# Kernel tuning notes

Hardware: AMD Instinct MI355X
Metric: run time of the kernel (lower is better)

Reference implementation:

```python
import jax, jax.numpy as jnp
import numpy as np

# dims: batch, seq, vocab, hidden, layers, heads, head_dim, intermediate
B, S, V, Hd, L, H, D, I = 2, 1024, 32000, 1024, 4, 16, 64, 4096
THETA = 1e6
EPS = 1e-6
TOPK = S // 2          # sparsity_ratio = 0.5 -> keep half of the keys per head
STD = 0.02
NEG = -1e9


def _ln(x, w, b):
    m = jnp.mean(x, -1, keepdims=True)
    v = jnp.mean((x - m) ** 2, -1, keepdims=True)
    return (x - m) * jax.lax.rsqrt(v + EPS) * w + b


def _rope_tables():
    inv = 1.0 / (THETA ** (np.arange(0, D, 2, dtype=np.float32) / D))
    f = np.arange(S, dtype=np.float32)[:, None] * inv[None, :]   # [S, D/2]
    emb = np.concatenate([f, f], -1)                              # [S, D]
    return jnp.asarray(np.cos(emb)), jnp.asarray(np.sin(emb))


def _rot(x):  # rotate-half, x: [B,H,S,D]
    x1, x2 = jnp.split(x, 2, axis=-1)
    return jnp.concatenate([-x2, x1], -1)


def setup_inputs() -> dict:
    key = jax.random.key(0)
    it = iter(jax.random.split(key, 24))
    p = lambda sh: jax.random.normal(next(it), sh, jnp.float32) * STD
    return {
        "input_ids": jax.random.randint(next(it), (B, S), 0, V, jnp.int32),
        "attention_mask": jnp.ones((B, S), jnp.float32),
        "embed": p((V, Hd)),
        "ln1_w": jnp.ones((L, Hd)), "ln1_b": jnp.zeros((L, Hd)),
        "Wq": p((L, Hd, Hd)), "Wk": p((L, Hd, Hd)),
        "Wv": p((L, Hd, Hd)), "Wo": p((L, Hd, Hd)),
        "Wr": p((L, Hd, H)),
        "ln2_w": jnp.ones((L, Hd)), "ln2_b": jnp.zeros((L, Hd)),
        "W1": p((L, Hd, I)), "b1": jnp.zeros((L, I)),
        "W2": p((L, I, Hd)), "b2": jnp.zeros((L, Hd)),
        "norm_w": jnp.ones((Hd,)), "norm_b": jnp.zeros((Hd,)),
        "lm_head": p((Hd, V)),
    }


def reference(input_ids, attention_mask, embed, ln1_w, ln1_b, Wq, Wk, Wv, Wo,
              Wr, ln2_w, ln2_b, W1, b1, W2, b2, norm_w, norm_b, lm_head):
    cos, sin = _rope_tables()                                   # [S, D]
    mask_add = (1.0 - attention_mask)[:, None, None, :] * NEG   # [B,1,1,S]
    x = embed[input_ids]                                        # [B,S,Hd]
    scale = 1.0 / np.sqrt(D)

    def block(x, p):
        h = _ln(x, p["ln1_w"], p["ln1_b"])
        heads = lambda w: jnp.einsum('bse,ed->bsd', h, w).reshape(B, S, H, D).transpose(0, 2, 1, 3)
        q, k, v = heads(p["Wq"]), heads(p["Wk"]), heads(p["Wv"])  # [B,H,S,D]
        q = q * cos + _rot(q) * sin
        k = k * cos + _rot(k) * sin
        router = jnp.einsum('bse,eh->bhs', h, p["Wr"])            # [B,H,S]
        kth = jax.lax.top_k(router, TOPK)[0][..., -1:]            # [B,H,1]
        bias = jnp.where(router >= kth, jax.nn.log_sigmoid(router), NEG)[:, :, None, :]
        logits = jnp.einsum('bhsd,bhtd->bhst', q, k) * scale + bias + mask_add
        attn = jax.nn.softmax(logits, -1)
        o = jnp.einsum('bhst,bhtd->bhsd', attn, v).transpose(0, 2, 1, 3).reshape(B, S, Hd)
        x = x + jnp.einsum('bse,ed->bsd', o, p["Wo"])
        h2 = _ln(x, p["ln2_w"], p["ln2_b"])
        m = jax.nn.silu(jnp.einsum('bse,ei->bsi', h2, p["W1"]) + p["b1"])
        x = x + jnp.einsum('bsi,ie->bse', m, p["W2"]) + p["b2"]
        return x, None

    layer_params = {"ln1_w": ln1_w, "ln1_b": ln1_b, "Wq": Wq, "Wk": Wk,
                    "Wv": Wv, "Wo": Wo, "Wr": Wr, "ln2_w": ln2_w,
                    "ln2_b": ln2_b, "W1": W1, "b1": b1, "W2": W2, "b2": b2}
    x, _ = jax.lax.scan(block, x, layer_params)
    x = _ln(x, norm_w, norm_b)
    return jnp.einsum('bse,ev->bsv', x, lm_head)   # [B,S,V]
```

## Files before the change

### kernel.cpp

```cpp
#include <hip/hip_runtime.h>
#include <hip/hip_bf16.h>

#define Bdim 2
#define Sdim 1024
#define Vdim 32000
#define HDdim 1024
#define Ldim 4
#define Hdim 16
#define Ddim 64
#define Idim 4096
#define BSdim 2048

typedef __attribute__((ext_vector_type(8))) short bf16x8;
typedef __attribute__((ext_vector_type(4))) float f32x4;

__device__ __forceinline__ unsigned short f2bf(float f) {
    __hip_bfloat16 h = __float2bfloat16(f);
    return *reinterpret_cast<unsigned short*>(&h);
}

#define MFMA16(a, b, c) __builtin_amdgcn_mfma_f32_16x16x32_bf16((a), (b), (c), 0, 0, 0)

#define GLD16(gp, lp)                                                            \
    __builtin_amdgcn_global_load_lds((const __attribute__((address_space(1))) void*)(gp), \
                                     (__attribute__((address_space(3))) void*)(lp), 16, 0, 0)

template <int N>
__device__ __forceinline__ void vwait() {
    if constexpr (N == 2) asm volatile("s_waitcnt vmcnt(2)" ::: "memory");
    else if constexpr (N == 3) asm volatile("s_waitcnt vmcnt(3)" ::: "memory");
    else if constexpr (N == 4) asm volatile("s_waitcnt vmcnt(4)" ::: "memory");
    else if constexpr (N == 6) asm volatile("s_waitcnt vmcnt(6)" ::: "memory");
}

__global__ __launch_bounds__(256) void tables_kernel(float* __restrict__ cosT, float* __restrict__ sinT) {
    int i = blockIdx.x * 256 + threadIdx.x;
    int d = i & 63;
    int s = i >> 6;
    float inv = powf(1.0e6f, -((float)(2 * (d & 31))) / 64.0f);
    float f = (float)s * inv;
    cosT[i] = cosf(f);
    sinT[i] = sinf(f);
}

__global__ __launch_bounds__(256) void embed_kernel(const int* __restrict__ ids, const float* __restrict__ emb,
                                                    float* __restrict__ x) {
    int m = blockIdx.x;
    int tid = threadIdx.x;
    int id = ids[m];
    const float4* src = (const float4*)(emb + (size_t)id * HDdim);
    ((float4*)(x + (size_t)m * HDdim))[tid] = src[tid];
}

__global__ __launch_bounds__(256) void ln_kernel(const float* __restrict__ x, const float* __restrict__ w,
                                                 const float* __restrict__ bw, unsigned short* __restrict__ outH,
                                                 const float* __restrict__ Wr, float* __restrict__ routerO) {
    int m = blockIdx.x;
    int tid = threadIdx.x;
    float4 a = ((const float4*)(x + (size_t)m * HDdim))[tid];
    float s = a.x + a.y + a.z + a.w;
    #pragma unroll
    for (int o = 1; o < 64; o <<= 1) s += __shfl_xor(s, o);
    __shared__ float red[4], red2[4];
    if ((tid & 63) == 0) red[tid >> 6] = s;
    __syncthreads();
    float mean = (red[0] + red[1] + red[2] + red[3]) * (1.0f / 1024.0f);
    float dx = a.x - mean, dy = a.y - mean, dz = a.z - mean, dw = a.w - mean;
    float s2 = dx * dx + dy * dy + dz * dz + dw * dw;
    #pragma unroll
    for (int o = 1; o < 64; o <<= 1) s2 += __shfl_xor(s2, o);
    if ((tid & 63) == 0) red2[tid >> 6] = s2;
    __syncthreads();
    float var = (red2[0] + red2[1] + red2[2] + red2[3]) * (1.0f / 1024.0f);
    float rs = rsqrtf(var + 1e-6f);
    float4 wv = ((const float4*)w)[tid];
    float4 bv = ((const float4*)bw)[tid];
    float v0 = dx * rs * wv.x + bv.x;
    float v1 = dy * rs * wv.y + bv.y;
    float v2 = dz * rs * wv.z + bv.z;
    float v3 = dw * rs * wv.w + bv.w;
    short4 st = make_short4((short)f2bf(v0), (short)f2bf(v1), (short)f2bf(v2), (short)f2bf(v3));
    *(short4*)(outH + (size_t)m * HDdim + tid * 4) = st;

    if (Wr) {
        __shared__ float rbuf[256][16];
        __shared__ float pbuf[16][17];
        float part[16];
        const float* wr0 = Wr + (size_t)(tid * 4) * Hdim;
        #pragma unroll
        for (int h = 0; h < 16; h++)
            part[h] = v0 * wr0[h] + v1 * wr0[16 + h] + v2 * wr0[32 + h] + v3 * wr0[48 + h];
        #pragma unroll
        for (int h4 = 0; h4 < 4; h4++)
            *(float4*)&rbuf[tid][h4 * 4] = make_float4(part[h4 * 4], part[h4 * 4 + 1], part[h4 * 4 + 2], part[h4 * 4 + 3]);
        __syncthreads();
        {
            int h = tid & 15, g = tid >> 4;
            float sgr = 0.0f;
            #pragma unroll
            for (int i = 0; i < 16; i++) sgr += rbuf[g * 16 + i][h];
            pbuf[g][h] = sgr;
        }
        __syncthreads();
        if (tid < 16) {
            float tot = 0.0f;
            #pragma unroll
            for (int g = 0; g < 16; g++) tot += pbuf[g][tid];
            int b = m >> 10, sI = m & 1023;
            routerO[((size_t)(b * Hdim + tid)) * Sdim + sI] = tot;
        }
    }
}

__global__ __launch_bounds__(1024) void topk_kernel(const float* __restrict__ router, const float* __restrict__ amask,
                                                    float* __restrict__ biasC, int* __restrict__ idxC,
                                                    int* __restrict__ ntA) {
    int bh = blockIdx.x;
    int t = threadIdx.x;
    __shared__ float r[1024];
    __shared__ float kths;
    __shared__ int wcnt[16];
    float v = router[(size_t)bh * Sdim + t];
    r[t] = v;
    __syncthreads();
    int gt = 0, eq = 0;
    for (int j = 0; j < 1024; j++) {
        float xv = r[j];
        gt += (xv > v) ? 1 : 0;
        eq += (xv == v) ? 1 : 0;
    }
    if (gt < 512 && gt + eq >= 512) kths = v;
    biasC[(size_t)bh * Sdim + t] = -1e9f;
    idxC[(size_t)bh * Sdim + t] = 0;
    __syncthreads();
    float kth = kths;
    bool sel = (v >= kth);
    unsigned long long m = __ballot(sel);
    int wid = t >> 6, lane = t & 63;
    if (lane == 0) wcnt[wid] = __popcll(m);
    __syncthreads();
    int base = 0;
    for (int w = 0; w < wid; w++) base += wcnt[w];
    if (sel) {
        int rank = base + (int)__popcll(m & ((1ull << lane) - 1ull));
        float bias = (v >= 0.0f) ? -log1pf(expf(-v)) : (v - log1pf(expf(v)));
        int b = bh >> 4;
        bias += (1.0f - amask[b * Sdim + t]) * (-1e9f);
        biasC[(size_t)bh * Sdim + rank] = bias;
        idxC[(size_t)bh * Sdim + rank] = t;
    }
    if (t == 0) {
        int tot = 0;
        #pragma unroll
        for (int w = 0; w < 16; w++) tot += wcnt[w];
        ntA[bh] = (tot + 63) >> 6;
    }
}

__global__ __launch_bounds__(256) void tconv_kernel(const float* __restrict__ S0,
                                                    unsigned short* __restrict__ D, int K, int ldS) {
    __shared__ float t[32][33];
    int kt = blockIdx.y * 32, nt = blockIdx.x * 32;
    int r = threadIdx.x >> 3, c4 = (threadIdx.x & 7) * 4;
    float4 v = *(const float4*)(S0 + (size_t)(kt + r) * ldS + nt + c4);
    t[r][c4] = v.x; t[r][c4 + 1] = v.y; t[r][c4 + 2] = v.z; t[r][c4 + 3] = v.w;
    __syncthreads();
    short4 o = make_short4((short)f2bf(t[c4][r]), (short)f2bf(t[c4 + 1][r]),
                           (short)f2bf(t[c4 + 2][r]), (short)f2bf(t[c4 + 3][r]));
    *(short4*)(D + (size_t)(nt + r) * K + kt + c4) = o;
}

__global__ __launch_bounds__(256) void tconv_layer(const float* __restrict__ Wq, const float* __restrict__ Wk,
                                                   const float* __restrict__ Wv, const float* __restrict__ Wo,
                                                   const float* __restrict__ W1, const float* __restrict__ W2,
                                                   unsigned short* __restrict__ wts) {
    const size_t M1 = 1u << 20;
    int bid = blockIdx.x;
    const float* S;
    unsigned short* D;
    int K, ldS, nt, kt;
    if (bid < 4096) {
        int z = bid >> 10, t = bid & 1023;
        S = (z == 0) ? Wq : (z == 1) ? Wk : (z == 2) ? Wv : Wo;
        D = wts + (size_t)z * M1;
        K = 1024; ldS = 1024; nt = t & 31; kt = t >> 5;
    } else if (bid < 8192) {
        int t = bid - 4096;
        S = W1; D = wts + 4 * M1;
        K = 1024; ldS = 4096; nt = t % 128; kt = t / 128;
    } else {
        int t = bid - 8192;
        S = W2; D = wts + 8 * M1;
        K = 4096; ldS = 1024; nt = t % 32; kt = t / 32;
    }
    __shared__ float tb[32][33];
    int ktb = kt * 32, ntb = nt * 32;
    int r = threadIdx.x >> 3, c4 = (threadIdx.x & 7) * 4;
    float4 v = *(const float4*)(S + (size_t)(ktb + r) * ldS + ntb + c4);
    tb[r][c4] = v.x; tb[r][c4 + 1] = v.y; tb[r][c4 + 2] = v.z; tb[r][c4 + 3] = v.w;
    __syncthreads();
    short4 o = make_short4((short)f2bf(tb[c4][r]), (short)f2bf(tb[c4 + 1][r]),
                           (short)f2bf(tb[c4 + 2][r]), (short)f2bf(tb[c4 + 3][r]));
    *(short4*)(D + (size_t)(ntb + r) * K + ktb + c4) = o;
}

__global__ __launch_bounds__(256) void kvgather_kernel(const unsigned short* __restrict__ k16,
                                                       const unsigned short* __restrict__ v16,
                                                       const int* __restrict__ idxC, const int* __restrict__ ntA,
                                                       unsigned short* __restrict__ kc,
                                                       unsigned short* __restrict__ vTc) {
    int jt = blockIdx.x;
    int bh = blockIdx.y;
    if (jt >= ntA[bh]) return;
    __shared__ unsigned short T[64][72];
    int tid = threadIdx.x;
    int jl = tid >> 2;
    int part = tid & 3;
    int j = jt * 64 + jl;
    int src = idxC[(size_t)bh * Sdim + j];
    const unsigned short* kr = k16 + ((size_t)bh * Sdim + src) * Ddim + part * 16;
    bf16x8 k0 = *(const bf16x8*)kr;
    bf16x8 k1 = *(const bf16x8*)(kr + 8);
    int swj = (j & 7) << 3;
    unsigned short* kd = kc + ((size_t)bh * Sdim + j) * Ddim;
    *(bf16x8*)(kd + ((part * 16) ^ swj)) = k0;
    *(bf16x8*)(kd + ((part * 16 + 8) ^ swj)) = k1;
    const unsigned short* vr = v16 + ((size_t)bh * Sdim + src) * Ddim + part * 16;
    *(bf16x8*)&T[jl][part * 16] = *(const bf16x8*)vr;
    *(bf16x8*)&T[jl][part * 16 + 8] = *(const bf16x8*)(vr + 8);
    __syncthreads();
    int d = tid >> 2;
    int xr = (d & 7) << 3;
    unsigned short* dst = vTc + ((size_t)bh * Ddim + d) * Sdim + jt * 64;
    #pragma unroll
    for (int cc = 0; cc < 2; cc++) {
        int tb = (tid & 3) * 16 + cc * 8;
        bf16x8 o;
        #pragma unroll
        for (int i = 0; i < 8; i++) o[i] = (short)T[tb + i][d];
        *(bf16x8*)(dst + (tb ^ xr)) = o;
    }
}

template <int EPI, int BM, int BN, int WM, int WN>
__global__ __launch_bounds__(512) void gemm8p(
    const unsigned short* __restrict__ A, const unsigned short* __restrict__ Bt,
    float* __restrict__ OF, unsigned short* __restrict__ Hq, unsigned short* __restrict__ Hk,
    unsigned short* __restrict__ Hv, const float* __restrict__ bias,
    const float* __restrict__ cosT, const float* __restrict__ sinT,
    int Kc, int ldK, int ldC, int gridM, int gridN) {
    constexpr int MI = BM / WM / 16, NI = BN / WN / 16;
    constexpr int MH = MI / 2, NH = NI / 2;
    constexpr int LA = BM / 128, LB = BN / 128;
    constexpr int HA = BM / WM / 2;
    constexpr int HB = BN / WN / 2;
    constexpr int ABUF = BM * 64, BBUF = BN * 64;

    __shared__ unsigned short lds[2 * ABUF + 2 * BBUF];

    int bid = blockIdx.x;
    const int nwg = gridDim.x;
    if ((nwg & 7) == 0) bid = (bid & 7) * (nwg >> 3) + (bid >> 3);
    const int mn = gridM * gridN;
    const int ks = bid / mn;
    const int rem = bid - ks * mn;
    const int bm = (rem % gridM) * BM;
    const int bn = (rem / gridM) * BN;
    const unsigned short* Ap = A + (size_t)ks * Kc;
    const unsigned short* Bp = Bt + (size_t)ks * Kc;

    const int tid = threadIdx.x;
    const int lane = tid & 63, wid = tid >> 6;
    const int lc = lane & 15, lg = lane >> 4;
    const int wwm = wid / WN, wwn = wid % WN;

    const int srow = tid >> 3;
    const int scol = ((tid & 7) ^ (srow & 7)) * 8;
    const int ak0 = (lg * 8) ^ ((lc & 7) * 8);
    const int ak1 = (32 + lg * 8) ^ ((lc & 7) * 8);

    f32x4 acc[MI][NI];
    f32x4 zero = {0.0f, 0.0f, 0.0f, 0.0f};
    #pragma unroll
    for (int i = 0; i < MI; i++)
        #pragma unroll
        for (int j = 0; j < NI; j++) acc[i][j] = zero;

    bf16x8 a[MH][2], b0[NH][2], b1[NH][2];

    auto stage_a = [&](int half, int nbuf, int kt) {
        #pragma unroll
        for (int j = 0; j < LA; j++) {
            const int idx = j * 64 + srow;
            const int grow = (idx / HA) * (BM / WM) + half * HA + (idx % HA);
            const unsigned short* g = Ap + (size_t)(bm + grow) * ldK + kt + scol;
            GLD16(g, &lds[nbuf * ABUF + half * (ABUF / 2) + (j * 512 + tid) * 8]);
        }
    };
    auto stage_b = [&](int half, int nbuf, int kt) {
        #pragma unroll
        for (int j = 0; j < LB; j++) {
            const int idx = j * 64 + srow;
            const int grow = (idx / HB) * (BN / WN) + half * HB + (idx % HB);
            const unsigned short* g = Bp + (size_t)(bn + grow) * ldK + kt + scol;
            GLD16(g, &lds[2 * ABUF + nbuf * BBUF + half * (BBUF / 2) + (j * 512 + tid) * 8]);
        }
    };

#define DS_A(mh_, cur_)                                                                   \
    _Pragma("unroll") for (int m = 0; m < MH; m++) {                                      \
        const int ro = (cur_)*ABUF + (mh_) * (ABUF / 2) + (wwm * HA + m * 16 + lc) * 64;  \
        a[m][0] = *(const bf16x8*)&lds[ro + ak0];                                         \
        a[m][1] = *(const bf16x8*)&lds[ro + ak1];                                         \
    }
#define DS_B(bb_, nh_, cur_)                                                              \
    _Pragma("unroll") for (int n = 0; n < NH; n++) {                                      \
        const int ro = 2 * ABUF + (cur_)*BBUF + (nh_) * (BBUF / 2) + (wwn * HB + n * 16 + lc) * 64; \
        bb_[n][0] = *(const bf16x8*)&lds[ro + ak0];                                       \
        bb_[n][1] = *(const bf16x8*)&lds[ro + ak1];                                       \
    }
#define MFMA_PH(mh_, nh_, bb_)                                                            \
    __builtin_amdgcn_s_setprio(1);                                                        \
    _Pragma("unroll") for (int m = 0; m < MH; m++) _Pragma("unroll") for (int n = 0; n < NH; n++) { \
        acc[(mh_)*MH + m][(nh_)*NH + n] = MFMA16(a[m][0], bb_[n][0], acc[(mh_)*MH + m][(nh_)*NH + n]); \
        acc[(mh_)*MH + m][(nh_)*NH + n] = MFMA16(a[m][1], bb_[n][1], acc[(mh_)*MH + m][(nh_)*NH + n]); \
    }                                                                                     \
    __builtin_amdgcn_s_setprio(0);
#define BAR_PRE()                                                                         \
    __builtin_amdgcn_sched_barrier(0);                                                    \
    __builtin_amdgcn_s_barrier();
#define BAR_END()                                                                         \
    asm volatile("" ::: "memory");                                                        \
    __builtin_amdgcn_s_barrier();                                                         \
    __builtin_amdgcn_sched_barrier(0);

    stage_a(0, 0, 0);
    stage_b(0, 0, 0);
    stage_b(1, 0, 0);
    stage_a(1, 0, 0);
    vwait<LA + LB>();
    BAR_END();

    const int NT = Kc >> 6;
    for (int t = 0; t < NT; t++) {
        const int cur = t & 1, nxt = cur ^ 1;
        const int ktn = (t + 1 < NT) ? (t + 1) * 64 : t * 64;
        DS_A(0, cur);
        DS_B(b0, 0, cur);
        stage_a(0, nxt, ktn);
        BAR_PRE();
        MFMA_PH(0, 0, b0);
        vwait<2 * LA>();
        BAR_END();
        DS_B(b1, 1, cur);
        stage_b(0, nxt, ktn);
        BAR_PRE();
        MFMA_PH(0, 1, b1);
        vwait<LA + LB>();
        BAR_END();
        DS_A(1, cur);
        stage_b(1, nxt, ktn);
        BAR_PRE();
        MFMA_PH(1, 1, b1);
        BAR_END();
        stage_a(1, nxt, ktn);
        BAR_PRE();
        MFMA_PH(1, 0, b0);
        vwait<LA + LB>();
        BAR_END();
    }
    asm volatile("s_waitcnt vmcnt(0)" ::: "memory");
#undef DS_A
#undef DS_B
#undef MFMA_PH
#undef BAR_PRE
#undef BAR_END

    #pragma unroll
    for (int i = 0; i < MI; i++) {
        if (EPI == 1) {
            const int colbase = bn + wwn * (BN / WN);
            const int zc = colbase >> 10;
            unsigned short* OH = (zc == 0) ? Hq : (zc == 1) ? Hk : Hv;
            const int hcol = (colbase >> 6) & 15;
            #pragma unroll
            for (int r = 0; r < 4; r++) {
                int row = bm + wwm * (BM / WM) + i * 16 + lg * 4 + r;
                int b = row >> 10, s = row & 1023;
                size_t base = ((size_t)(b * Hdim + hcol) * Sdim + s) << 6;
                if (zc == 2) {
                    #pragma unroll
                    for (int j = 0; j < 4; j++) OH[base + j * 16 + lc] = f2bf(acc[i][j][r]);
                } else {
                    #pragma unroll
                    for (int j = 0; j < 2; j++) {
                        int d = j * 16 + lc;
                        float x1 = acc[i][j][r];
                        float x2 = acc[i][j + 2][r];
                        float c = cosT[s * 64 + d];
                        float sn = sinT[s * 64 + d];
                        OH[base + d] = f2bf(x1 * c - x2 * sn);
                        OH[base + d + 32] = f2bf(x2 * c + x1 * sn);
                    }
                }
            }
        } else {
            #pragma unroll
            for (int r = 0; r < 4; r++) {
                int row = bm + wwm * (BM / WM) + i * 16 + lg * 4 + r;
                #pragma unroll
                for (int j = 0; j < NI; j++) {
                    int col = bn + wwn * (BN / WN) + j * 16 + lc;
                    float v = acc[i][j][r];
                    if (EPI == 3) {
                        float t = v + bias[col];
                        Hq[(size_t)row * ldC + col] = f2bf(t / (1.0f + expf(-t)));
                    } else if (EPI == 6) {
                        if (ks == 0 && bias != nullptr) v += bias[col];
                        unsafeAtomicAdd(&OF[(size_t)row * ldC + col], v);
                    } else {
                        OF[(size_t)row * ldC + col] = v;
                    }
                }
            }
        }
    }
}

__global__ __launch_bounds__(256) void attn_kernel(const unsigned short* __restrict__ q16,
                                                   const unsigned short* __restrict__ kc,
                                                   const unsigned short* __restrict__ vTc,
                                                   const float* __restrict__ biasC,
                                                   const int* __restrict__ ntA,
                                                   unsigned short* __restrict__ o16) {
    const int qb = blockIdx.x;
    const int bh = blockIdx.y;
    const int tid = threadIdx.x;
    const int w = tid >> 6, lane = tid & 63;
    const int lg = lane >> 4, lc = lane & 15;
    const int nt = ntA[bh];

    __shared__ unsigned short Ks[2][64 * 64];
    __shared__ unsigned short Vs[2][64 * 64];
    __shared__ unsigned short Pq[4][16][72];
    __shared__ float sbAll[1024];

    {
        const float4 bv = ((const float4*)(biasC + (size_t)bh * Sdim))[tid];
        *(float4*)&sbAll[tid * 4] = bv;
    }

    const int qrow = qb * 64 + w * 16 + lc;
    const unsigned short* qbase = q16 + ((size_t)bh * Sdim + qrow) * Ddim;
    bf16x8 qf[2];
    qf[0] = *(const bf16x8*)(qbase + lg * 8);
    qf[1] = *(const bf16x8*)(qbase + 32 + lg * 8);

    const int grow = tid >> 3;
    const int gc = (tid & 7) * 8;
    const unsigned short* kbase = kc + (size_t)bh * Sdim * Ddim;
    const unsigned short* vbase = vTc + (size_t)bh * Ddim * Sdim;

    {
        const unsigned short* kg = kbase + (size_t)grow * Ddim + gc;
        GLD16(kg, &Ks[0][tid * 8]);
        GLD16(kg + 32 * Ddim, &Ks[0][2048 + tid * 8]);
        const unsigned short* vg = vbase + (size_t)grow * Sdim + gc;
        GLD16(vg, &Vs[0][tid * 8]);
        GLD16(vg + 32 * Sdim, &Vs[0][2048 + tid * 8]);
    }
    __syncthreads();

    float m_i = -1e30f, l_i = 0.0f;
    f32x4 ot[4];
    f32x4 zero = {0.0f, 0.0f, 0.0f, 0.0f};
    #pragma unroll
    for (int fd = 0; fd < 4; fd++) ot[fd] = zero;

    const int sw = (lc & 7) << 3;

    for (int tt = 0; tt < nt; tt++) {
        const int cur = tt & 1;
        if (tt > 0) {
            asm volatile("s_waitcnt vmcnt(0)" ::: "memory");
            __builtin_amdgcn_sched_barrier(0);
            __builtin_amdgcn_s_barrier();
        }
        if (tt < nt - 1) {
            const int t1 = (tt + 1) * 64;
            const unsigned short* kg = kbase + (size_t)(t1 + grow) * Ddim + gc;
            GLD16(kg, &Ks[cur ^ 1][tid * 8]);
            GLD16(kg + 32 * Ddim, &Ks[cur ^ 1][2048 + tid * 8]);
            const unsigned short* vg = vbase + (size_t)grow * Sdim + t1 + gc;
            GLD16(vg, &Vs[cur ^ 1][tid * 8]);
            GLD16(vg + 32 * Sdim, &Vs[cur ^ 1][2048 + tid * 8]);
        }

        f32x4 sf[4];
        #pragma unroll
        for (int f = 0; f < 4; f++) {
            const int trow = f * 16 + lc;
            f32x4 a = zero;
            #pragma unroll
            for (int ks = 0; ks < 2; ks++) {
                bf16x8 kfr = *(bf16x8*)&Ks[cur][trow * 64 + ((ks * 32 + lg * 8) ^ sw)];
                a = MFMA16(kfr, qf[ks], a);
            }
            sf[f] = a;
        }
        const int t0 = tt * 64;
        float tmax = -1e30f;
        #pragma unroll
        for (int f = 0; f < 4; f++)
            #pragma unroll
            for (int j = 0; j < 4; j++) {
                float v = sf[f][j] * 0.125f + sbAll[t0 + f * 16 + lg * 4 + j];
                sf[f][j] = v;
                tmax = fmaxf(tmax, v);
            }
        tmax = fmaxf(tmax, __shfl_xor(tmax, 16));
        tmax = fmaxf(tmax, __shfl_xor(tmax, 32));
        float mnew = fmaxf(m_i, tmax);
        float alpha = expf(m_i - mnew);
        float lsum = 0.0f;
        #pragma unroll
        for (int f = 0; f < 4; f++)
            #pragma unroll
            for (int j = 0; j < 4; j++) {
                float p = expf(sf[f][j] - mnew);
                sf[f][j] = p;
                lsum += p;
            }
        lsum += __shfl_xor(lsum, 16);
        lsum += __shfl_xor(lsum, 32);
        l_i = l_i * alpha + lsum;
        m_i = mnew;
        #pragma unroll
        for (int fd = 0; fd < 4; fd++)
            #pragma unroll
            for (int j = 0; j < 4; j++) ot[fd][j] *= alpha;
        #pragma unroll
        for (int f = 0; f < 4; f++) {
            short4 ps = make_short4((short)f2bf(sf[f][0]), (short)f2bf(sf[f][1]),
                                    (short)f2bf(sf[f][2]), (short)f2bf(sf[f][3]));
            *(short4*)&Pq[w][lc][f * 16 + lg * 4] = ps;
        }
        #pragma unroll
        for (int ks = 0; ks < 2; ks++) {
            bf16x8 pf = *(bf16x8*)&Pq[w][lc][ks * 32 + lg * 8];
            #pragma unroll
            for (int fd = 0; fd < 4; fd++) {
                bf16x8 vfr = *(bf16x8*)&Vs[cur][(fd * 16 + lc) * 64 + ((ks * 32 + lg * 8) ^ sw)];
                ot[fd] = MFMA16(vfr, pf, ot[fd]);
            }
        }
    }
    asm volatile("s_waitcnt vmcnt(0)" ::: "memory");
    float rl = 1.0f / l_i;
    int b = bh >> 4, h = bh & 15;
    #pragma unroll
    for (int fd = 0; fd < 4; fd++)
        #pragma unroll
        for (int j = 0; j < 4; j++) {
            int d = fd * 16 + lg * 4 + j;
            o16[((size_t)b * Sdim + qrow) * HDdim + h * 64 + d] = f2bf(ot[fd][j] * rl);
        }
}

extern "C" void kernel_launch(void* const* d_in, const int* in_sizes, int n_in,
                              void* d_out, int out_size, void* d_ws, size_t ws_size,
                              hipStream_t stream) {
    const int* ids = (const int*)d_in[0];
    const float* amask = (const float*)d_in[1];
    const float* emb = (const float*)d_in[2];
    const float* ln1w = (const float*)d_in[3];
    const float* ln1b = (const float*)d_in[4];
    const float* Wq = (const float*)d_in[5];
    const float* Wk = (const float*)d_in[6];
    const float* Wv = (const float*)d_in[7];
    const float* Wo = (const float*)d_in[8];
    const float* Wr = (const float*)d_in[9];
    const float* ln2w = (const float*)d_in[10];
    const float* ln2b = (const float*)d_in[11];
    const float* W1 = (const float*)d_in[12];
    const float* b1 = (const float*)d_in[13];
    const float* W2 = (const float*)d_in[14];
    const float* b2 = (const float*)d_in[15];
    const float* nw = (const float*)d_in[16];
    const float* nb = (const float*)d_in[17];
    const float* lmh = (const float*)d_in[18];
    float* out = (float*)d_out;

    char* p = (char*)d_ws;
    size_t off = 0;
    auto alloc = [&](size_t bytes) -> void* {
        void* r = p + off;
        off += (bytes + 255) & ~(size_t)255;
        return r;
    };
    float* cosT = (float*)alloc((size_t)Sdim * Ddim * 4);
    float* sinT = (float*)alloc((size_t)Sdim * Ddim * 4);
    float* x = (float*)alloc((size_t)BSdim * HDdim * 4);
    unsigned short* h16 = (unsigned short*)alloc((size_t)BSdim * HDdim * 2);
    unsigned short* o16 = (unsigned short*)alloc((size_t)BSdim * HDdim * 2);
    unsigned short* m16 = (unsigned short*)alloc((size_t)BSdim * Idim * 2);
    unsigned short* q16 = (unsigned short*)alloc((size_t)Bdim * Hdim * Sdim * Ddim * 2);
    unsigned short* k16 = (unsigned short*)alloc((size_t)Bdim * Hdim * Sdim * Ddim * 2);
    unsigned short* v16 = (unsigned short*)alloc((size_t)Bdim * Hdim * Sdim * Ddim * 2);
    unsigned short* kcs = (unsigned short*)alloc((size_t)Bdim * Hdim * Sdim * Ddim * 2);
    unsigned short* vTc = (unsigned short*)alloc((size_t)Bdim * Hdim * Sdim * Ddim * 2);
    float* router = (float*)alloc((size_t)Bdim * Hdim * Sdim * 4);
    float* biasC = (float*)alloc((size_t)Bdim * Hdim * Sdim * 4);
    int* idxC = (int*)alloc((size_t)Bdim * Hdim * Sdim * 4);
    int* ntA = (int*)alloc((size_t)Bdim * Hdim * 4);
    unsigned short* wts = (unsigned short*)alloc((size_t)Vdim * HDdim * 2);

    const size_t M1 = 1u << 20;

    tables_kernel<<<256, 256, 0, stream>>>(cosT, sinT);
    embed_kernel<<<BSdim, 256, 0, stream>>>(ids, emb, x);

    for (int l = 0; l < Ldim; l++) {
        const float* Wq_l = Wq + (size_t)l * HDdim * HDdim;
        const float* Wk_l = Wk + (size_t)l * HDdim * HDdim;
        const float* Wv_l = Wv + (size_t)l * HDdim * HDdim;
        const float* Wo_l = Wo + (size_t)l * HDdim * HDdim;
        const float* Wr_l = Wr + (size_t)l * HDdim * Hdim;
        const float* W1_l = W1 + (size_t)l * HDdim * Idim;
        const float* W2_l = W2 + (size_t)l * Idim * HDdim;
        const float* b1_l = b1 + (size_t)l * Idim;
        const float* b2_l = b2 + (size_t)l * HDdim;

        tconv_layer<<<12288, 256, 0, stream>>>(Wq_l, Wk_l, Wv_l, Wo_l, W1_l, W2_l, wts);

        ln_kernel<<<BSdim, 256, 0, stream>>>(x, ln1w + l * HDdim, ln1b + l * HDdim, h16, Wr_l, router);
        topk_kernel<<<Bdim * Hdim, 1024, 0, stream>>>(router, amask, biasC, idxC, ntA);
        gemm8p<1, 128, 128, 4, 2><<<384, 512, 0, stream>>>(h16, wts, nullptr, q16, k16, v16,
                                                           nullptr, cosT, sinT, HDdim, HDdim, 0, 16, 24);
        kvgather_kernel<<<dim3(16, 32), 256, 0, stream>>>(k16, v16, idxC, ntA, kcs, vTc);
        attn_kernel<<<dim3(16, 32), 256, 0, stream>>>(q16, kcs, vTc, biasC, ntA, o16);
        gemm8p<6, 128, 128, 4, 2><<<256, 512, 0, stream>>>(o16, wts + 3 * M1, x, nullptr, nullptr, nullptr,
                                                           nullptr, nullptr, nullptr, 512, HDdim, HDdim, 16, 8);
        ln_kernel<<<BSdim, 256, 0, stream>>>(x, ln2w + l * HDdim, ln2b + l * HDdim, h16, nullptr, nullptr);
        gemm8p<3, 128, 128, 4, 2><<<512, 512, 0, stream>>>(h16, wts + 4 * M1, nullptr, m16, nullptr, nullptr,
                                                           b1_l, nullptr, nullptr, HDdim, HDdim, Idim, 16, 32);
        gemm8p<6, 128, 128, 4, 2><<<512, 512, 0, stream>>>(m16, wts + 8 * M1, x, nullptr, nullptr, nullptr,
                                                           b2_l, nullptr, nullptr, 1024, Idim, HDdim, 16, 8);
    }

    ln_kernel<<<BSdim, 256, 0, stream>>>(x, nw, nb, h16, nullptr, nullptr);
    tconv_kernel<<<dim3(1000, 32, 1), 256, 0, stream>>>(lmh, wts, HDdim, Vdim);
    gemm8p<5, 128, 128, 4, 2><<<4000, 512, 0, stream>>>(h16, wts, out, nullptr, nullptr, nullptr,
                                                        nullptr, nullptr, nullptr, HDdim, HDdim, Vdim, 16, 250);
}
```

Baseline: 1.036 ms.

## Batch weight conversion, gather K inside attention, enlarge LM-head GEMM tiles

All per-layer weight transposes and the lm_head transpose now run up front as one batched conversion into a per-layer buffer, so the per-layer tconv launches are gone. The K gather is folded into the attention kernel, which loads selected key rows by index straight into LDS, so the separate compacted K copy is no longer written and re-read. The LM-head GEMM switches to 256x256 tiles with a 2x4 wave layout. The new buffer costs extra memory, and the bigger tiles may hurt occupancy or register pressure.

```diff
diff --git a/kernel.cpp b/kernel.cpp
--- a/kernel.cpp
+++ b/kernel.cpp
@@ -170,27 +170,29 @@
     *(short4*)(D + (size_t)(nt + r) * K + kt + c4) = o;
 }
 
-__global__ __launch_bounds__(256) void tconv_layer(const float* __restrict__ Wq, const float* __restrict__ Wk,
-                                                   const float* __restrict__ Wv, const float* __restrict__ Wo,
-                                                   const float* __restrict__ W1, const float* __restrict__ W2,
-                                                   unsigned short* __restrict__ wts) {
+__global__ __launch_bounds__(256) void tconv_all(const float* __restrict__ Wq, const float* __restrict__ Wk,
+                                                 const float* __restrict__ Wv, const float* __restrict__ Wo,
+                                                 const float* __restrict__ W1, const float* __restrict__ W2,
+                                                 unsigned short* __restrict__ wtsL) {
     const size_t M1 = 1u << 20;
     int bid = blockIdx.x;
+    int lid = bid / 12288, sub = bid - lid * 12288;
+    unsigned short* wl = wtsL + (size_t)lid * 12 * M1;
     const float* S;
     unsigned short* D;
     int K, ldS, nt, kt;
-    if (bid < 4096) {
-        int z = bid >> 10, t = bid & 1023;
-        S = (z == 0) ? Wq : (z == 1) ? Wk : (z == 2) ? Wv : Wo;
-        D = wts + (size_t)z * M1;
+    if (sub < 4096) {
+        int z = sub >> 10, t = sub & 1023;
+        S = ((z == 0) ? Wq : (z == 1) ? Wk : (z == 2) ? Wv : Wo) + (size_t)lid * M1;
+        D = wl + (size_t)z * M1;
         K = 1024; ldS = 1024; nt = t & 31; kt = t >> 5;
-    } else if (bid < 8192) {
-        int t = bid - 4096;
-        S = W1; D = wts + 4 * M1;
+    } else if (sub < 8192) {
+        int t = sub - 4096;
+        S = W1 + (size_t)lid * 4 * M1; D = wl + 4 * M1;
         K = 1024; ldS = 4096; nt = t % 128; kt = t / 128;
     } else {
-        int t = bid - 8192;
-        S = W2; D = wts + 8 * M1;
+        int t = sub - 8192;
+        S = W2 + (size_t)lid * 4 * M1; D = wl + 8 * M1;
         K = 4096; ldS = 1024; nt = t % 32; kt = t / 32;
     }
     __shared__ float tb[32][33];
@@ -204,11 +206,9 @@
     *(short4*)(D + (size_t)(ntb + r) * K + ktb + c4) = o;
 }
 
-__global__ __launch_bounds__(256) void kvgather_kernel(const unsigned short* __restrict__ k16,
-                                                       const unsigned short* __restrict__ v16,
-                                                       const int* __restrict__ idxC, const int* __restrict__ ntA,
-                                                       unsigned short* __restrict__ kc,
-                                                       unsigned short* __restrict__ vTc) {
+__global__ __launch_bounds__(256) void vgather_kernel(const unsigned short* __restrict__ v16,
+                                                      const int* __restrict__ idxC, const int* __restrict__ ntA,
+                                                      unsigned short* __restrict__ vTc) {
     int jt = blockIdx.x;
     int bh = blockIdx.y;
     if (jt >= ntA[bh]) return;
@@ -218,13 +218,6 @@
     int part = tid & 3;
     int j = jt * 64 + jl;
     int src = idxC[(size_t)bh * Sdim + j];
-    const unsigned short* kr = k16 + ((size_t)bh * Sdim + src) * Ddim + part * 16;
-    bf16x8 k0 = *(const bf16x8*)kr;
-    bf16x8 k1 = *(const bf16x8*)(kr + 8);
-    int swj = (j & 7) << 3;
-    unsigned short* kd = kc + ((size_t)bh * Sdim + j) * Ddim;
-    *(bf16x8*)(kd + ((part * 16) ^ swj)) = k0;
-    *(bf16x8*)(kd + ((part * 16 + 8) ^ swj)) = k1;
     const unsigned short* vr = v16 + ((size_t)bh * Sdim + src) * Ddim + part * 16;
     *(bf16x8*)&T[jl][part * 16] = *(const bf16x8*)vr;
     *(bf16x8*)&T[jl][part * 16 + 8] = *(const bf16x8*)(vr + 8);
@@ -428,8 +421,9 @@
 }
 
 __global__ __launch_bounds__(256) void attn_kernel(const unsigned short* __restrict__ q16,
-                                                   const unsigned short* __restrict__ kc,
+                                                   const unsigned short* __restrict__ k16,
                                                    const unsigned short* __restrict__ vTc,
+                                                   const int* __restrict__ idxC,
                                                    const float* __restrict__ biasC,
                                                    const int* __restrict__ ntA,
                                                    unsigned short* __restrict__ o16) {
@@ -458,13 +452,20 @@
 
     const int grow = tid >> 3;
     const int gc = (tid & 7) * 8;
-    const unsigned short* kbase = kc + (size_t)bh * Sdim * Ddim;
+    const int ksw = (grow & 7) << 3;
+    const unsigned short* kbase = k16 + (size_t)bh * Sdim * Ddim;
+    const int* ibase = idxC + (size_t)bh * Sdim;
     const unsigned short* vbase = vTc + (size_t)bh * Ddim * Sdim;
 
+    auto stageK = [&](int buf, int t1) {
+        int s0 = ibase[t1 + grow];
+        int s1 = ibase[t1 + 32 + grow];
+        GLD16(kbase + (size_t)s0 * Ddim + (gc ^ ksw), &Ks[buf][tid * 8]);
+        GLD16(kbase + (size_t)s1 * Ddim + (gc ^ ksw), &Ks[buf][2048 + tid * 8]);
+    };
+
     {
-        const unsigned short* kg = kbase + (size_t)grow * Ddim + gc;
-        GLD16(kg, &Ks[0][tid * 8]);
-        GLD16(kg + 32 * Ddim, &Ks[0][2048 + tid * 8]);
+        stageK(0, 0);
         const unsigned short* vg = vbase + (size_t)grow * Sdim + gc;
         GLD16(vg, &Vs[0][tid * 8]);
         GLD16(vg + 32 * Sdim, &Vs[0][2048 + tid * 8]);
@@ -488,9 +489,7 @@
         }
         if (tt < nt - 1) {
             const int t1 = (tt + 1) * 64;
-            const unsigned short* kg = kbase + (size_t)(t1 + grow) * Ddim + gc;
-            GLD16(kg, &Ks[cur ^ 1][tid * 8]);
-            GLD16(kg + 32 * Ddim, &Ks[cur ^ 1][2048 + tid * 8]);
+            stageK(cur ^ 1, t1);
             const unsigned short* vg = vbase + (size_t)grow * Sdim + t1 + gc;
             GLD16(vg, &Vs[cur ^ 1][tid * 8]);
             GLD16(vg + 32 * Sdim, &Vs[cur ^ 1][2048 + tid * 8]);
@@ -607,49 +606,43 @@
     unsigned short* q16 = (unsigned short*)alloc((size_t)Bdim * Hdim * Sdim * Ddim * 2);
     unsigned short* k16 = (unsigned short*)alloc((size_t)Bdim * Hdim * Sdim * Ddim * 2);
     unsigned short* v16 = (unsigned short*)alloc((size_t)Bdim * Hdim * Sdim * Ddim * 2);
-    unsigned short* kcs = (unsigned short*)alloc((size_t)Bdim * Hdim * Sdim * Ddim * 2);
     unsigned short* vTc = (unsigned short*)alloc((size_t)Bdim * Hdim * Sdim * Ddim * 2);
     float* router = (float*)alloc((size_t)Bdim * Hdim * Sdim * 4);
     float* biasC = (float*)alloc((size_t)Bdim * Hdim * Sdim * 4);
     int* idxC = (int*)alloc((size_t)Bdim * Hdim * Sdim * 4);
     int* ntA = (int*)alloc((size_t)Bdim * Hdim * 4);
     unsigned short* wts = (unsigned short*)alloc((size_t)Vdim * HDdim * 2);
+    unsigned short* wtsL = (unsigned short*)alloc((size_t)Ldim * 12 * (1u << 20) * 2);
 
     const size_t M1 = 1u << 20;
 
     tables_kernel<<<256, 256, 0, stream>>>(cosT, sinT);
     embed_kernel<<<BSdim, 256, 0, stream>>>(ids, emb, x);
+    tconv_kernel<<<dim3(1000, 32, 1), 256, 0, stream>>>(lmh, wts, HDdim, Vdim);
+    tconv_all<<<Ldim * 12288, 256, 0, stream>>>(Wq, Wk, Wv, Wo, W1, W2, wtsL);
 
     for (int l = 0; l < Ldim; l++) {
-        const float* Wq_l = Wq + (size_t)l * HDdim * HDdim;
-        const float* Wk_l = Wk + (size_t)l * HDdim * HDdim;
-        const float* Wv_l = Wv + (size_t)l * HDdim * HDdim;
-        const float* Wo_l = Wo + (size_t)l * HDdim * HDdim;
+        unsigned short* wl = wtsL + (size_t)l * 12 * M1;
         const float* Wr_l = Wr + (size_t)l * HDdim * Hdim;
-        const float* W1_l = W1 + (size_t)l * HDdim * Idim;
-        const float* W2_l = W2 + (size_t)l * Idim * HDdim;
         const float* b1_l = b1 + (size_t)l * Idim;
         const float* b2_l = b2 + (size_t)l * HDdim;
 
-        tconv_layer<<<12288, 256, 0, stream>>>(Wq_l, Wk_l, Wv_l, Wo_l, W1_l, W2_l, wts);
-
         ln_kernel<<<BSdim, 256, 0, stream>>>(x, ln1w + l * HDdim, ln1b + l * HDdim, h16, Wr_l, router);
         topk_kernel<<<Bdim * Hdim, 1024, 0, stream>>>(router, amask, biasC, idxC, ntA);
-        gemm8p<1, 128, 128, 4, 2><<<384, 512, 0, stream>>>(h16, wts, nullptr, q16, k16, v16,
+        gemm8p<1, 128, 128, 4, 2><<<384, 512, 0, stream>>>(h16, wl, nullptr, q16, k16, v16,
                                                            nullptr, cosT, sinT, HDdim, HDdim, 0, 16, 24);
-        kvgather_kernel<<<dim3(16, 32), 256, 0, stream>>>(k16, v16, idxC, ntA, kcs, vTc);
-        attn_kernel<<<dim3(16, 32), 256, 0, stream>>>(q16, kcs, vTc, biasC, ntA, o16);
-        gemm8p<6, 128, 128, 4, 2><<<256, 512, 0, stream>>>(o16, wts + 3 * M1, x, nullptr, nullptr, nullptr,
+        vgather_kernel<<<dim3(16, 32), 256, 0, stream>>>(v16, idxC, ntA, vTc);
+        attn_kernel<<<dim3(16, 32), 256, 0, stream>>>(q16, k16, vTc, idxC, biasC, ntA, o16);
+        gemm8p<6, 128, 128, 4, 2><<<256, 512, 0, stream>>>(o16, wl + 3 * M1, x, nullptr, nullptr, nullptr,
                                                            nullptr, nullptr, nullptr, 512, HDdim, HDdim, 16, 8);
         ln_kernel<<<BSdim, 256, 0, stream>>>(x, ln2w + l * HDdim, ln2b + l * HDdim, h16, nullptr, nullptr);
-        gemm8p<3, 128, 128, 4, 2><<<512, 512, 0, stream>>>(h16, wts + 4 * M1, nullptr, m16, nullptr, nullptr,
+        gemm8p<3, 128, 128, 4, 2><<<512, 512, 0, stream>>>(h16, wl + 4 * M1, nullptr, m16, nullptr, nullptr,
                                                            b1_l, nullptr, nullptr, HDdim, HDdim, Idim, 16, 32);
-        gemm8p<6, 128, 128, 4, 2><<<512, 512, 0, stream>>>(m16, wts + 8 * M1, x, nullptr, nullptr, nullptr,
+        gemm8p<6, 128, 128, 4, 2><<<512, 512, 0, stream>>>(m16, wl + 8 * M1, x, nullptr, nullptr, nullptr,
                                                            b2_l, nullptr, nullptr, 1024, Idim, HDdim, 16, 8);
     }
 
     ln_kernel<<<BSdim, 256, 0, stream>>>(x, nw, nb, h16, nullptr, nullptr);
-    tconv_kernel<<<dim3(1000, 32, 1), 256, 0, stream>>>(lmh, wts, HDdim, Vdim);
-    gemm8p<5, 128, 128, 4, 2><<<4000, 512, 0, stream>>>(h16, wts, out, nullptr, nullptr, nullptr,
-                                                        nullptr, nullptr, nullptr, HDdim, HDdim, Vdim, 16, 250);
-}
+    gemm8p<5, 256, 256, 2, 4><<<1000, 512, 0, stream>>>(h16, wts, out, nullptr, nullptr, nullptr,
+                                                        nullptr, nullptr, nullptr, HDdim, HDdim, Vdim, 8, 125);
+}
```

New measurement: 1.028 ms. No clear change (-0.8%).
